# Optimization experiments

Hardware: AMD Instinct MI355X
Metric: run time of the kernel (lower is better)

The kernel has to match this reference:

```python
import jax, jax.numpy as jnp
import numpy as np

RULE = 110
NUM_NEIGHBOURS = 1
N_SIZE = 1 + 2 * NUM_NEIGHBOURS  # 3
ITERATIONS = 64
THRESHOLD = 0.5
WRAP = False


def setup_inputs() -> dict:
    key = jax.random.key(0)
    x = jax.random.uniform(key, (32, 16384), dtype=jnp.float32)
    # lookup[k] = k-th base-2 digit of rule  (Ca1ReplaceRules.lookup)
    lookup = jnp.array([(RULE >> k) & 1 for k in range(2 ** N_SIZE)], dtype=jnp.int32)
    return {"x": x, "lookup": lookup}


def reference(x, lookup):
    batch, width = x.shape
    width_n = (width // N_SIZE + 1) * N_SIZE
    pad_right = N_SIZE + width_n - width - 1  # padded width = width_n + N_SIZE - 1 + 1
    # threshold float input to binary states (lookup dtype is integer in torch)
    state0 = (x >= THRESHOLD).astype(jnp.int32)

    def step(state, _):
        if WRAP:
            padded = jnp.pad(state, ((0, 0), (1, pad_right)), mode="wrap")
        else:
            padded = jnp.pad(state, ((0, 0), (1, pad_right)))
        # idx[b, j] = sum_n padded[b, j+n] * 2**n  (sliding window of size N_SIZE)
        idx = jnp.zeros((batch, width_n), jnp.int32)
        for n in range(N_SIZE):
            idx = idx + padded[:, n:n + width_n] * (2 ** n)
        new = jnp.take(lookup, idx, axis=0)[:, :width]
        return new, new

    _, hist = jax.lax.scan(step, state0, None, length=ITERATIONS)
    full = jnp.concatenate([state0[None], hist], axis=0)  # [iters+1, B, W]
    return jnp.transpose(full, (1, 0, 2))  # [B, iters+1, W]
```

## Files before the change

kernel.cpp:

```cpp
#include <hip/hip_runtime.h>
#include <stdint.h>


#define WIDTH   16384
#define BATCH   32
#define ITERS   64
#define WORDS64 (WIDTH / 64)
#define WPL     4

__global__ __launch_bounds__(64) void ca_steps_kernel(
    const float* __restrict__ x, uint64_t* __restrict__ packed)
{
    const int b    = blockIdx.x;
    const int lane = threadIdx.x;

    const float* xb = x + (size_t)b * WIDTH;

    uint64_t c[WPL];
    const float4* xv = (const float4*)(xb + lane * 256);
    #pragma unroll
    for (int k = 0; k < WPL; ++k) {
        uint64_t m = 0;
        #pragma unroll
        for (int i = 0; i < 16; ++i) {
            float4 f = xv[k * 16 + i];
            m |= (uint64_t)(f.x >= 0.5f) << (i * 4 + 0);
            m |= (uint64_t)(f.y >= 0.5f) << (i * 4 + 1);
            m |= (uint64_t)(f.z >= 0.5f) << (i * 4 + 2);
            m |= (uint64_t)(f.w >= 0.5f) << (i * 4 + 3);
        }
        c[k] = m;
    }

    uint64_t* pb = packed + ((size_t)b * (ITERS + 1)) * WORDS64 + (size_t)lane * WPL;

    #pragma unroll
    for (int k = 0; k < WPL; ++k) pb[k] = c[k];

    for (int t = 1; t <= ITERS; ++t) {
        uint64_t A = __ballot((c[0] & 1ull) != 0);
        uint64_t B = __ballot((c[WPL - 1] >> 63) != 0);
        uint64_t carryL = ((B << 1) >> lane) & 1ull;
        uint64_t carryR = ((A >> 1) >> lane) & 1ull;

        uint64_t l0 = (c[0] << 1) | carryL;
        uint64_t l1 = (c[1] << 1) | (c[0] >> 63);
        uint64_t l2 = (c[2] << 1) | (c[1] >> 63);
        uint64_t l3 = (c[3] << 1) | (c[2] >> 63);

        uint64_t r0 = (c[0] >> 1) | (c[1] << 63);
        uint64_t r1 = (c[1] >> 1) | (c[2] << 63);
        uint64_t r2 = (c[2] >> 1) | (c[3] << 63);
        uint64_t r3 = (c[3] >> 1) | (carryR << 63);

        c[0] = (l0 | c[0]) & ~(l0 & c[0] & r0);
        c[1] = (l1 | c[1]) & ~(l1 & c[1] & r1);
        c[2] = (l2 | c[2]) & ~(l2 & c[2] & r2);
        c[3] = (l3 | c[3]) & ~(l3 & c[3] & r3);

        uint64_t* pt = pb + (size_t)t * WORDS64;
        #pragma unroll
        for (int k = 0; k < WPL; ++k) pt[k] = c[k];
    }
}

__global__ __launch_bounds__(256) void unpack_kernel(
    const uint32_t* __restrict__ packed, int4* __restrict__ out, int n4)
{
    int g = blockIdx.x * 256 + threadIdx.x;
    if (g >= n4) return;
    uint32_t w   = packed[g >> 3];
    uint32_t nib = w >> ((g & 7) * 4);
    out[g] = make_int4((int)(nib & 1u), (int)((nib >> 1) & 1u),
                       (int)((nib >> 2) & 1u), (int)((nib >> 3) & 1u));
}

extern "C" void kernel_launch(void* const* d_in, const int* in_sizes, int n_in,
                              void* d_out, int out_size, void* d_ws, size_t ws_size,
                              hipStream_t stream)
{
    const float* x = (const float*)d_in[0];

    uint64_t* packed = (uint64_t*)d_ws;

    ca_steps_kernel<<<BATCH, 64, 0, stream>>>(x, packed);

    const int n4 = BATCH * (ITERS + 1) * (WIDTH / 4);
    unpack_kernel<<<(n4 + 255) / 256, 256, 0, stream>>>(
        (const uint32_t*)d_ws, (int4*)d_out, n4);
}
```

Before: 150.6 us.

## Fuse CA stepping and unpacking into one tiled kernel with halo recomputation

Replaces the two-kernel scheme (bit-packed stepping into a workspace, then a separate unpack pass) with a single kernel. It tiles the width into 1024-cell tiles with a 64-cell halo on each side and recomputes the halo, giving 16x more blocks. Each step's state is unpacked straight to the int32 output through shared memory, which removes the workspace round trip and the second launch. In exchange it adds redundant halo computation and two barriers per iteration. Correctness now depends on the halo being wide enough for 64 steps.

```diff
diff --git a/kernel.cpp b/kernel.cpp
--- a/kernel.cpp
+++ b/kernel.cpp
@@ -2,77 +2,65 @@
 #include <stdint.h>
 
 
-#define WIDTH   16384
-#define BATCH   32
-#define ITERS   64
-#define WORDS64 (WIDTH / 64)
-#define WPL     4
+#define WIDTH 16384
+#define BATCH 32
+#define ITERS 64
+#define TILE  1024
+#define NTILE (WIDTH / TILE)
 
-__global__ __launch_bounds__(64) void ca_steps_kernel(
-    const float* __restrict__ x, uint64_t* __restrict__ packed)
+__global__ __launch_bounds__(64) void ca_fused_kernel(
+    const float* __restrict__ x, int* __restrict__ out)
 {
-    const int b    = blockIdx.x;
     const int lane = threadIdx.x;
+    const int tile = blockIdx.x;
+    const int b    = blockIdx.y;
+    const int s    = tile * TILE;
 
-    const float* xb = x + (size_t)b * WIDTH;
+    __shared__ uint32_t sh[64];
 
-    uint64_t c[WPL];
-    const float4* xv = (const float4*)(xb + lane * 256);
-    #pragma unroll
-    for (int k = 0; k < WPL; ++k) {
-        uint64_t m = 0;
+    const int p0 = s - 64 + lane * 32;
+    const bool valid = (p0 >= 0) && (p0 < WIDTH);
+    const uint32_t vmask = valid ? 0xffffffffu : 0u;
+
+    uint32_t c = 0;
+    if (valid) {
+        const float4* xv = (const float4*)(x + (size_t)b * WIDTH + p0);
         #pragma unroll
-        for (int i = 0; i < 16; ++i) {
-            float4 f = xv[k * 16 + i];
-            m |= (uint64_t)(f.x >= 0.5f) << (i * 4 + 0);
-            m |= (uint64_t)(f.y >= 0.5f) << (i * 4 + 1);
-            m |= (uint64_t)(f.z >= 0.5f) << (i * 4 + 2);
-            m |= (uint64_t)(f.w >= 0.5f) << (i * 4 + 3);
+        for (int i = 0; i < 8; ++i) {
+            float4 f = xv[i];
+            c |= (uint32_t)(f.x >= 0.5f) << (i * 4 + 0);
+            c |= (uint32_t)(f.y >= 0.5f) << (i * 4 + 1);
+            c |= (uint32_t)(f.z >= 0.5f) << (i * 4 + 2);
+            c |= (uint32_t)(f.w >= 0.5f) << (i * 4 + 3);
         }
-        c[k] = m;
     }
 
-    uint64_t* pb = packed + ((size_t)b * (ITERS + 1)) * WORDS64 + (size_t)lane * WPL;
+    int* outb = out + ((size_t)b * (ITERS + 1)) * WIDTH + s;
 
-    #pragma unroll
-    for (int k = 0; k < WPL; ++k) pb[k] = c[k];
+    for (int t = 0; t <= ITERS; ++t) {
+        sh[lane] = c;
+        __syncthreads();
+        int4* ov = (int4*)outb;
+        #pragma unroll
+        for (int j = 0; j < 4; ++j) {
+            uint32_t w   = sh[2 + j * 8 + (lane >> 3)];
+            uint32_t nib = w >> ((lane & 7) * 4);
+            ov[j * 64 + lane] = make_int4((int)(nib & 1u), (int)((nib >> 1) & 1u),
+                                          (int)((nib >> 2) & 1u), (int)((nib >> 3) & 1u));
+        }
+        __syncthreads();
+        outb += WIDTH;
+        if (t == ITERS) break;
 
-    for (int t = 1; t <= ITERS; ++t) {
-        uint64_t A = __ballot((c[0] & 1ull) != 0);
-        uint64_t B = __ballot((c[WPL - 1] >> 63) != 0);
-        uint64_t carryL = ((B << 1) >> lane) & 1ull;
-        uint64_t carryR = ((A >> 1) >> lane) & 1ull;
+        uint64_t A  = __ballot((c & 1u) != 0);
+        uint64_t Bm = __ballot((c >> 31) != 0);
+        uint32_t carryL = (uint32_t)(((Bm << 1) >> lane) & 1ull);
+        uint32_t carryR = (uint32_t)(((A  >> 1) >> lane) & 1ull);
 
-        uint64_t l0 = (c[0] << 1) | carryL;
-        uint64_t l1 = (c[1] << 1) | (c[0] >> 63);
-        uint64_t l2 = (c[2] << 1) | (c[1] >> 63);
-        uint64_t l3 = (c[3] << 1) | (c[2] >> 63);
-
-        uint64_t r0 = (c[0] >> 1) | (c[1] << 63);
-        uint64_t r1 = (c[1] >> 1) | (c[2] << 63);
-        uint64_t r2 = (c[2] >> 1) | (c[3] << 63);
-        uint64_t r3 = (c[3] >> 1) | (carryR << 63);
-
-        c[0] = (l0 | c[0]) & ~(l0 & c[0] & r0);
-        c[1] = (l1 | c[1]) & ~(l1 & c[1] & r1);
-        c[2] = (l2 | c[2]) & ~(l2 & c[2] & r2);
-        c[3] = (l3 | c[3]) & ~(l3 & c[3] & r3);
-
-        uint64_t* pt = pb + (size_t)t * WORDS64;
-        #pragma unroll
-        for (int k = 0; k < WPL; ++k) pt[k] = c[k];
+        uint32_t l = (c << 1) | carryL;
+        uint32_t r = (c >> 1) | (carryR << 31);
+        c = ((l | c) & ~(l & c & r)) & vmask;
     }
-}
-
-__global__ __launch_bounds__(256) void unpack_kernel(
-    const uint32_t* __restrict__ packed, int4* __restrict__ out, int n4)
-{
-    int g = blockIdx.x * 256 + threadIdx.x;
-    if (g >= n4) return;
-    uint32_t w   = packed[g >> 3];
-    uint32_t nib = w >> ((g & 7) * 4);
-    out[g] = make_int4((int)(nib & 1u), (int)((nib >> 1) & 1u),
-                       (int)((nib >> 2) & 1u), (int)((nib >> 3) & 1u));
 }
 
 extern "C" void kernel_launch(void* const* d_in, const int* in_sizes, int n_in,
@@ -80,12 +68,8 @@
                               hipStream_t stream)
 {
     const float* x = (const float*)d_in[0];
+    (void)d_ws; (void)ws_size;
 
-    uint64_t* packed = (uint64_t*)d_ws;
-
-    ca_steps_kernel<<<BATCH, 64, 0, stream>>>(x, packed);
-
-    const int n4 = BATCH * (ITERS + 1) * (WIDTH / 4);
-    unpack_kernel<<<(n4 + 255) / 256, 256, 0, stream>>>(
-        (const uint32_t*)d_ws, (int4*)d_out, n4);
+    dim3 grid(NTILE, BATCH);
+    ca_fused_kernel<<<grid, 64, 0, stream>>>(x, (int*)d_out);
 }
```

Measured after the change: 137.5 us. 1.1x faster.
